# Optimization experiments

Hardware: AMD Instinct MI355X
Metric: run time of the kernel (lower is better)

The kernel has to match this reference:

```python
import jax, jax.numpy as jnp
import numpy as np
import math

LAMBDA_INIT = 0.8 - 0.6 * math.exp(-0.3 * 2)  # depth=2


def setup_inputs() -> dict:
    key = jax.random.key(0)
    ks = jax.random.split(key, 10)
    B, T, E, hd = 1, 2048, 1024, 32
    s = 0.02
    return {
        "x": jax.random.normal(ks[0], (B, T, E), jnp.float32),
        "Wq": jax.random.normal(ks[1], (E, E), jnp.float32) * s,
        "Wk": jax.random.normal(ks[2], (E, E), jnp.float32) * s,
        "Wv": jax.random.normal(ks[3], (E, E), jnp.float32) * s,
        "Wo": jax.random.normal(ks[4], (E, E), jnp.float32) * s,
        "lambda_q1": jax.random.normal(ks[5], (hd,), jnp.float32) * 0.1,
        "lambda_k1": jax.random.normal(ks[6], (hd,), jnp.float32) * 0.1,
        "lambda_q2": jax.random.normal(ks[7], (hd,), jnp.float32) * 0.1,
        "lambda_k2": jax.random.normal(ks[8], (hd,), jnp.float32) * 0.1,
        "gamma": jnp.ones((2 * hd,), jnp.float32),
    }


def reference(x, Wq, Wk, Wv, Wo, lambda_q1, lambda_k1, lambda_q2, lambda_k2, gamma):
    B, T, E = x.shape
    hd = gamma.shape[0] // 2          # head_dim
    H = E // (2 * hd)                 # num_heads
    scaling = hd ** -0.5

    # projections (torch Linear: y = x @ W.T)
    q = (x @ Wq.T).reshape(B, T, 2 * H, hd).transpose(0, 2, 1, 3)  # [B,2H,T,hd]
    k = (x @ Wk.T).reshape(B, T, 2 * H, hd).transpose(0, 2, 1, 3)  # [B,2H,T,hd]
    v = (x @ Wv.T).reshape(B, T, H, 2 * hd).transpose(0, 2, 1, 3)  # [B,H,T,2hd]

    # causal mask (offset = 0 since src_len == tgt_len)
    mask = jnp.triu(jnp.full((T, T), -jnp.inf, jnp.float32), k=1)

    attn_weights = jnp.einsum('bhtd,bhsd->bhts', q * scaling, k) + mask
    attn_weights = jax.nn.softmax(attn_weights.astype(jnp.float32), axis=-1).astype(x.dtype)

    lambda_1 = jnp.exp(jnp.sum(lambda_q1 * lambda_k1).astype(jnp.float32))
    lambda_2 = jnp.exp(jnp.sum(lambda_q2 * lambda_k2).astype(jnp.float32))
    lambda_full = (lambda_1 - lambda_2 + LAMBDA_INIT).astype(x.dtype)

    aw = attn_weights.reshape(B, H, 2, T, T)
    diff = aw[:, :, 0] - lambda_full * aw[:, :, 1]          # [B,H,T,T]

    attn = jnp.einsum('bhts,bhsd->bhtd', diff, v)            # [B,H,T,2hd]

    # RMSNorm over last dim (computed in fp32)
    a32 = attn.astype(jnp.float32)
    normed = a32 * jax.lax.rsqrt(jnp.mean(a32 * a32, axis=-1, keepdims=True) + 1e-5)
    attn = gamma * normed.astype(attn.dtype)
    attn = attn * (1 - LAMBDA_INIT)

    attn = attn.transpose(0, 2, 1, 3).reshape(B, T, E)
    return attn @ Wo.T
```

## Files before the change

### kernel.cpp

```cpp
#include <hip/hip_runtime.h>
#include <math.h>

typedef float f32x4 __attribute__((ext_vector_type(4)));
typedef __bf16 bf16x8 __attribute__((ext_vector_type(8)));

#define MFMA16(a, b, c) __builtin_amdgcn_mfma_f32_16x16x32_bf16((a), (b), (c), 0, 0, 0)

__device__ __forceinline__ unsigned short f2bf(float f) {
    union { float f; unsigned u; } v; v.f = f;
    return (unsigned short)((v.u + 0x7fffu + ((v.u >> 16) & 1u)) >> 16);
}
__device__ __forceinline__ unsigned pack2(float a, float b) {
    return (unsigned)f2bf(a) | ((unsigned)f2bf(b) << 16);
}

__global__ __launch_bounds__(256)
void convert_bf16(const float* __restrict__ x,  const float* __restrict__ wq,
                  const float* __restrict__ wk, const float* __restrict__ wv,
                  const float* __restrict__ wo,
                  unsigned short* __restrict__ xb,  unsigned short* __restrict__ wqb,
                  unsigned short* __restrict__ wkb, unsigned short* __restrict__ wvb,
                  unsigned short* __restrict__ wob)
{
    int i = blockIdx.x * 256 + threadIdx.x;
    const float* s; unsigned short* d; int o;
    if (i < 524288)       { s = x;  d = xb;  o = i; }
    else if (i < 786432)  { s = wq; d = wqb; o = i - 524288; }
    else if (i < 1048576) { s = wk; d = wkb; o = i - 786432; }
    else if (i < 1310720) { s = wv; d = wvb; o = i - 1048576; }
    else                  { s = wo; d = wob; o = i - 1310720; }
    float4 v = *reinterpret_cast<const float4*>(s + (size_t)o * 4);
    ushort4 r;
    r.x = f2bf(v.x); r.y = f2bf(v.y); r.z = f2bf(v.z); r.w = f2bf(v.w);
    *reinterpret_cast<ushort4*>(d + (size_t)o * 4) = r;
}

__device__ __forceinline__ void gemm_bf16_body(const unsigned short* __restrict__ A,
                                               const unsigned short* __restrict__ W,
                                               void* __restrict__ Cp, int mode)
{
    __shared__ char Al[128 * 128];
    __shared__ char Bl[64 * 128];

    const int tid = threadIdx.x;
    const int lane = tid & 63, w = tid >> 6;
    const int g = lane >> 4, r15 = lane & 15;
    const int wm = (w >> 1) * 64, wn = (w & 1) * 32;
    const int m0 = blockIdx.y * 128, n0 = blockIdx.x * 64;

    f32x4 acc[4][2] = {};
    bf16x8 ra[4], rb[2];

#pragma unroll
    for (int p = 0; p < 4; p++) {
        int idx = p * 256 + tid;
        int row = idx >> 3, c8 = idx & 7;
        ra[p] = *reinterpret_cast<const bf16x8*>(A + (size_t)(m0 + row) * 1024 + c8 * 8);
    }
#pragma unroll
    for (int p = 0; p < 2; p++) {
        int idx = p * 256 + tid;
        int row = idx >> 3, c8 = idx & 7;
        rb[p] = *reinterpret_cast<const bf16x8*>(W + (size_t)(n0 + row) * 1024 + c8 * 8);
    }

    for (int k0 = 0; k0 < 1024; k0 += 64) {
        __syncthreads();
#pragma unroll
        for (int p = 0; p < 4; p++) {
            int idx = p * 256 + tid;
            int row = idx >> 3, c8 = idx & 7;
            int byte = (row * 128 + c8 * 16) ^ ((row & 7) << 4);
            *reinterpret_cast<bf16x8*>(Al + byte) = ra[p];
        }
#pragma unroll
        for (int p = 0; p < 2; p++) {
            int idx = p * 256 + tid;
            int row = idx >> 3, c8 = idx & 7;
            int byte = (row * 128 + c8 * 16) ^ ((row & 7) << 4);
            *reinterpret_cast<bf16x8*>(Bl + byte) = rb[p];
        }
        if (k0 + 64 < 1024) {
#pragma unroll
            for (int p = 0; p < 4; p++) {
                int idx = p * 256 + tid;
                int row = idx >> 3, c8 = idx & 7;
                ra[p] = *reinterpret_cast<const bf16x8*>(A + (size_t)(m0 + row) * 1024 + k0 + 64 + c8 * 8);
            }
#pragma unroll
            for (int p = 0; p < 2; p++) {
                int idx = p * 256 + tid;
                int row = idx >> 3, c8 = idx & 7;
                rb[p] = *reinterpret_cast<const bf16x8*>(W + (size_t)(n0 + row) * 1024 + k0 + 64 + c8 * 8);
            }
        }
        __syncthreads();
#pragma unroll
        for (int c = 0; c < 2; c++) {
            bf16x8 af[4], bfr[2];
#pragma unroll
            for (int m = 0; m < 4; m++) {
                int row = wm + m * 16 + r15;
                int byte = (row * 128 + g * 16 + c * 64) ^ ((row & 7) << 4);
                af[m] = *reinterpret_cast<const bf16x8*>(Al + byte);
            }
#pragma unroll
            for (int n = 0; n < 2; n++) {
                int row = wn + n * 16 + r15;
                int byte = (row * 128 + g * 16 + c * 64) ^ ((row & 7) << 4);
                bfr[n] = *reinterpret_cast<const bf16x8*>(Bl + byte);
            }
#pragma unroll
            for (int m = 0; m < 4; m++)
#pragma unroll
                for (int n = 0; n < 2; n++)
                    acc[m][n] = MFMA16(af[m], bfr[n], acc[m][n]);
        }
    }

    if (mode == 0 || mode == 3) {
        const float cs = (mode == 3) ? 0.25504190132624806f : 1.0f;
        unsigned short* C = (unsigned short*)Cp;
#pragma unroll
        for (int m = 0; m < 4; m++)
#pragma unroll
            for (int n = 0; n < 2; n++)
#pragma unroll
                for (int i = 0; i < 4; i++)
                    C[(size_t)(m0 + wm + m * 16 + g * 4 + i) * 1024 + n0 + wn + n * 16 + r15] =
                        f2bf(acc[m][n][i] * cs);
    } else if (mode == 1) {
        unsigned short* C = (unsigned short*)Cp;
#pragma unroll
        for (int m = 0; m < 4; m++)
#pragma unroll
            for (int n = 0; n < 2; n++) {
                unsigned long long v = (unsigned long long)pack2(acc[m][n][0], acc[m][n][1])
                                     | ((unsigned long long)pack2(acc[m][n][2], acc[m][n][3]) << 32);
                *reinterpret_cast<unsigned long long*>(
                    C + (size_t)(n0 + wn + n * 16 + r15) * 2048 + m0 + wm + m * 16 + g * 4) = v;
            }
    } else {
        float* C = (float*)Cp;
#pragma unroll
        for (int m = 0; m < 4; m++)
#pragma unroll
            for (int n = 0; n < 2; n++)
#pragma unroll
                for (int i = 0; i < 4; i++)
                    C[(size_t)(m0 + wm + m * 16 + g * 4 + i) * 1024 + n0 + wn + n * 16 + r15] =
                        acc[m][n][i];
    }
}

__global__ __launch_bounds__(256)
void gemm_qkv_bf16(const unsigned short* __restrict__ xb, const unsigned short* __restrict__ wqb,
                   const unsigned short* __restrict__ wkb, const unsigned short* __restrict__ wvb,
                   unsigned short* __restrict__ Qb, unsigned short* __restrict__ Kb,
                   unsigned short* __restrict__ Vtb)
{
    int z = blockIdx.z;
    const unsigned short* W = (z == 0) ? wqb : (z == 1) ? wkb : wvb;
    void* C = (z == 0) ? (void*)Qb : (z == 1) ? (void*)Kb : (void*)Vtb;
    gemm_bf16_body(xb, W, C, (z == 2) ? 1 : (z == 0 ? 3 : 0));
}

__global__ __launch_bounds__(256)
void gemm_out_bf16(const unsigned short* __restrict__ Nb, const unsigned short* __restrict__ wob,
                   float* __restrict__ out)
{
    gemm_bf16_body(Nb, wob, out, 2);
}

__global__ __launch_bounds__(64, 3)
void attn_mfma3(const unsigned short* __restrict__ Qb, const unsigned short* __restrict__ Kb,
                const unsigned short* __restrict__ Vtb, unsigned short* __restrict__ Nb,
                const float* __restrict__ lq1, const float* __restrict__ lk1,
                const float* __restrict__ lq2, const float* __restrict__ lk2,
                const float* __restrict__ gamma)
{
    __shared__ char Pl[2][16 * 128];

    const int lane = threadIdx.x;
    const int g = lane >> 4, r15 = lane & 15;
    const int u = blockIdx.x >> 4, h = blockIdx.x & 15;
    const int qb = 127 - u;
    const int q0 = qb * 16;
    const int row_g = q0 + r15;

    float s1 = 0.f, s2 = 0.f;
#pragma unroll
    for (int i = 0; i < 32; i++) { s1 += lq1[i] * lk1[i]; s2 += lq2[i] * lk2[i]; }
    const float LI = 0.4707130183435841f;
    const float lam = expf(s1) - expf(s2) + LI;

    bf16x8 qf0 = *reinterpret_cast<const bf16x8*>(Qb + (size_t)row_g * 1024 + h * 64 + g * 8);
    bf16x8 qf1 = *reinterpret_cast<const bf16x8*>(Qb + (size_t)row_g * 1024 + h * 64 + 32 + g * 8);

    const unsigned short* Kh = Kb + h * 64;
    const unsigned short* Vh = Vtb + (size_t)(h * 64) * 2048;

    f32x4 oacc[2][4] = {};
    float m_u[2] = {-INFINITY, -INFINITY};
    float l_l[2] = {0.f, 0.f};

    const int nkb = (q0 + 79) >> 6;
    for (int kb = 0; kb < nkb; kb++) {
        const int j0 = kb * 64;

        bf16x8 ka0[4], ka1[4];
#pragma unroll
        for (int m = 0; m < 4; m++) {
            const unsigned short* kp = Kh + (size_t)(j0 + m * 16 + r15) * 1024 + g * 8;
            ka0[m] = *reinterpret_cast<const bf16x8*>(kp);
            ka1[m] = *reinterpret_cast<const bf16x8*>(kp + 32);
        }
        bf16x8 vf[4][2];
#pragma unroll
        for (int n = 0; n < 4; n++) {
            const unsigned short* vp = Vh + (size_t)(n * 16 + r15) * 2048 + j0 + g * 8;
            vf[n][0] = *reinterpret_cast<const bf16x8*>(vp);
            vf[n][1] = *reinterpret_cast<const bf16x8*>(vp + 32);
        }

        f32x4 sc0[4] = {}, sc1[4] = {};
#pragma unroll
        for (int m = 0; m < 4; m++) {
            sc0[m] = MFMA16(ka0[m], qf0, sc0[m]);
            sc1[m] = MFMA16(ka1[m], qf1, sc1[m]);
        }

        const bool diag = (kb == nkb - 1);
#pragma unroll
        for (int s = 0; s < 2; s++) {
            f32x4* sc = s ? sc1 : sc0;
            float sv[4][4];
            float mxl = -INFINITY;
            if (diag) {
#pragma unroll
                for (int m = 0; m < 4; m++)
#pragma unroll
                    for (int i = 0; i < 4; i++) {
                        float xv = ((j0 + m * 16 + g * 4 + i) <= row_g) ? sc[m][i] : -INFINITY;
                        sv[m][i] = xv;
                        mxl = fmaxf(mxl, xv);
                    }
            } else {
#pragma unroll
                for (int m = 0; m < 4; m++)
#pragma unroll
                    for (int i = 0; i < 4; i++) {
                        sv[m][i] = sc[m][i];
                        mxl = fmaxf(mxl, sc[m][i]);
                    }
            }
            if (__any(mxl > m_u[s] + 8.0f)) {
                float wm = mxl;
                wm = fmaxf(wm, __shfl_xor(wm, 1));
                wm = fmaxf(wm, __shfl_xor(wm, 2));
                wm = fmaxf(wm, __shfl_xor(wm, 4));
                wm = fmaxf(wm, __shfl_xor(wm, 8));
                wm = fmaxf(wm, __shfl_xor(wm, 16));
                wm = fmaxf(wm, __shfl_xor(wm, 32));
                const float corr = exp2f(m_u[s] - wm);
                m_u[s] = wm;
                l_l[s] *= corr;
#pragma unroll
                for (int n = 0; n < 4; n++)
#pragma unroll
                    for (int i = 0; i < 4; i++) oacc[s][n][i] *= corr;
            }
            float sum = 0.f;
#pragma unroll
            for (int m = 0; m < 4; m++) {
                float p0 = exp2f(sv[m][0] - m_u[s]);
                float p1 = exp2f(sv[m][1] - m_u[s]);
                float p2 = exp2f(sv[m][2] - m_u[s]);
                float p3 = exp2f(sv[m][3] - m_u[s]);
                sum += (p0 + p1) + (p2 + p3);
                unsigned long long pv = (unsigned long long)pack2(p0, p1)
                                      | ((unsigned long long)pack2(p2, p3) << 32);
                int byte = (r15 * 128 + m * 32 + g * 8) ^ ((r15 & 7) << 4);
                *reinterpret_cast<unsigned long long*>(Pl[s] + byte) = pv;
            }
            l_l[s] += sum;
        }

#pragma unroll
        for (int c = 0; c < 2; c++) {
            int pb = (r15 * 128 + g * 16 + c * 64) ^ ((r15 & 7) << 4);
            bf16x8 p0 = *reinterpret_cast<const bf16x8*>(Pl[0] + pb);
            bf16x8 p1 = *reinterpret_cast<const bf16x8*>(Pl[1] + pb);
#pragma unroll
            for (int n = 0; n < 4; n++) {
                oacc[0][n] = MFMA16(p0, vf[n][c], oacc[0][n]);
                oacc[1][n] = MFMA16(p1, vf[n][c], oacc[1][n]);
            }
        }
    }

    float l0 = l_l[0];
    l0 += __shfl_xor(l0, 16); l0 += __shfl_xor(l0, 32);
    float l1 = l_l[1];
    l1 += __shfl_xor(l1, 16); l1 += __shfl_xor(l1, 32);
    const float r1 = 1.f / l0;
    const float r2 = lam / l1;
    float i1[4], i2[4];
#pragma unroll
    for (int i = 0; i < 4; i++) {
        i1[i] = __shfl(r1, g * 4 + i);
        i2[i] = __shfl(r2, g * 4 + i);
    }
    float o[4][4], ss[4] = {0.f, 0.f, 0.f, 0.f};
#pragma unroll
    for (int n = 0; n < 4; n++)
#pragma unroll
        for (int i = 0; i < 4; i++) {
            float v = oacc[0][n][i] * i1[i] - oacc[1][n][i] * i2[i];
            o[n][i] = v;
            ss[i] = fmaf(v, v, ss[i]);
        }
#pragma unroll
    for (int i = 0; i < 4; i++) {
        ss[i] += __shfl_xor(ss[i], 1);
        ss[i] += __shfl_xor(ss[i], 2);
        ss[i] += __shfl_xor(ss[i], 4);
        ss[i] += __shfl_xor(ss[i], 8);
    }
    const float post = 1.f - LI;
    float gm4[4];
#pragma unroll
    for (int n = 0; n < 4; n++) gm4[n] = gamma[n * 16 + r15];
#pragma unroll
    for (int i = 0; i < 4; i++) {
        const float rs = rsqrtf(ss[i] * 0.015625f + 1e-5f);
#pragma unroll
        for (int n = 0; n < 4; n++) {
            Nb[(size_t)(q0 + g * 4 + i) * 1024 + h * 64 + n * 16 + r15] =
                f2bf(o[n][i] * rs * gm4[n] * post);
        }
    }
}

extern "C" void kernel_launch(void* const* d_in, const int* in_sizes, int n_in,
                              void* d_out, int out_size, void* d_ws, size_t ws_size,
                              hipStream_t stream)
{
    const float* x   = (const float*)d_in[0];
    const float* Wq  = (const float*)d_in[1];
    const float* Wk  = (const float*)d_in[2];
    const float* Wv  = (const float*)d_in[3];
    const float* Wo  = (const float*)d_in[4];
    const float* lq1 = (const float*)d_in[5];
    const float* lk1 = (const float*)d_in[6];
    const float* lq2 = (const float*)d_in[7];
    const float* lk2 = (const float*)d_in[8];
    const float* gm  = (const float*)d_in[9];
    float* out = (float*)d_out;

    unsigned short* ws  = (unsigned short*)d_ws;
    unsigned short* xb  = ws;
    unsigned short* wqb = xb  + 2097152;
    unsigned short* wkb = wqb + 1048576;
    unsigned short* wvb = wkb + 1048576;
    unsigned short* wob = wvb + 1048576;
    unsigned short* Qb  = wob + 1048576;
    unsigned short* Kb  = Qb  + 2097152;
    unsigned short* Vtb = Kb  + 2097152;
    unsigned short* Nb  = Vtb + 2097152;

    convert_bf16<<<6144, 256, 0, stream>>>(x, Wq, Wk, Wv, Wo, xb, wqb, wkb, wvb, wob);
    gemm_qkv_bf16<<<dim3(16, 16, 3), 256, 0, stream>>>(xb, wqb, wkb, wvb, Qb, Kb, Vtb);
    attn_mfma3<<<2048, 64, 0, stream>>>(Qb, Kb, Vtb, Nb, lq1, lk1, lq2, lk2, gm);
    gemm_out_bf16<<<dim3(16, 16), 256, 0, stream>>>(Nb, wob, out);
}
```

Before: 197.3 us.

## Prefetch next K tile in attention loop and use hardware bf16 pack

Restructures the attention kernel's key loop into a ping-pong, two-tile unrolled form. The next tile's K fragments are loaded into registers while the current tile's softmax and PV MFMAs run, hiding global load latency. It also swaps the software round-to-nearest bf16 packing for the v_cvt_pk_bf16_f32 instruction and lowers the launch-bounds occupancy hint from 3 to 2 waves. The trade is higher register pressure from the double-buffered K fragments and possibly lower occupancy.

```diff
diff --git a/kernel.cpp b/kernel.cpp
--- a/kernel.cpp
+++ b/kernel.cpp
@@ -12,6 +12,11 @@
 }
 __device__ __forceinline__ unsigned pack2(float a, float b) {
     return (unsigned)f2bf(a) | ((unsigned)f2bf(b) << 16);
+}
+__device__ __forceinline__ unsigned cvtpk_bf16(float lo, float hi) {
+    unsigned r;
+    asm("v_cvt_pk_bf16_f32 %0, %1, %2" : "=v"(r) : "v"(lo), "v"(hi));
+    return r;
 }
 
 __global__ __launch_bounds__(256)
@@ -172,8 +177,117 @@
     gemm_bf16_body(Nb, wob, out, 2);
 }
 
-__global__ __launch_bounds__(64, 3)
-void attn_mfma3(const unsigned short* __restrict__ Qb, const unsigned short* __restrict__ Kb,
+struct AttnState {
+    f32x4 oacc[2][4];
+    float m_u[2];
+    float l_l[2];
+};
+
+__device__ __forceinline__ void attn_tile(
+    int t, int nkb, int row_g, int g, int r15,
+    const unsigned short* __restrict__ Kh, const unsigned short* __restrict__ Vh,
+    bf16x8 (&kc0)[4], bf16x8 (&kc1)[4],
+    bf16x8 (&kn0)[4], bf16x8 (&kn1)[4],
+    const bf16x8& qf0, const bf16x8& qf1,
+    AttnState& st, char* __restrict__ Pl0, char* __restrict__ Pl1)
+{
+    const int j0 = t * 64;
+
+    bf16x8 vf[4][2];
+#pragma unroll
+    for (int n = 0; n < 4; n++) {
+        const unsigned short* vp = Vh + (size_t)(n * 16 + r15) * 2048 + j0 + g * 8;
+        vf[n][0] = *reinterpret_cast<const bf16x8*>(vp);
+        vf[n][1] = *reinterpret_cast<const bf16x8*>(vp + 32);
+    }
+
+    f32x4 sc0[4] = {}, sc1[4] = {};
+#pragma unroll
+    for (int m = 0; m < 4; m++) {
+        sc0[m] = MFMA16(kc0[m], qf0, sc0[m]);
+        sc1[m] = MFMA16(kc1[m], qf1, sc1[m]);
+    }
+
+    const int jn = ((t + 1 < nkb) ? t + 1 : t) * 64;
+#pragma unroll
+    for (int m = 0; m < 4; m++) {
+        const unsigned short* kp = Kh + (size_t)(jn + m * 16 + r15) * 1024 + g * 8;
+        kn0[m] = *reinterpret_cast<const bf16x8*>(kp);
+        kn1[m] = *reinterpret_cast<const bf16x8*>(kp + 32);
+    }
+
+    const bool diag = (t == nkb - 1);
+#pragma unroll
+    for (int s = 0; s < 2; s++) {
+        f32x4* sc = s ? sc1 : sc0;
+        char* Pl = s ? Pl1 : Pl0;
+        float sv[4][4];
+        float mxl = -INFINITY;
+        if (diag) {
+#pragma unroll
+            for (int m = 0; m < 4; m++)
+#pragma unroll
+                for (int i = 0; i < 4; i++) {
+                    float xv = ((j0 + m * 16 + g * 4 + i) <= row_g) ? sc[m][i] : -INFINITY;
+                    sv[m][i] = xv;
+                    mxl = fmaxf(mxl, xv);
+                }
+        } else {
+#pragma unroll
+            for (int m = 0; m < 4; m++)
+#pragma unroll
+                for (int i = 0; i < 4; i++) {
+                    sv[m][i] = sc[m][i];
+                    mxl = fmaxf(mxl, sc[m][i]);
+                }
+        }
+        if (__any(mxl > st.m_u[s] + 8.0f)) {
+            float wm = mxl;
+            wm = fmaxf(wm, __shfl_xor(wm, 1));
+            wm = fmaxf(wm, __shfl_xor(wm, 2));
+            wm = fmaxf(wm, __shfl_xor(wm, 4));
+            wm = fmaxf(wm, __shfl_xor(wm, 8));
+            wm = fmaxf(wm, __shfl_xor(wm, 16));
+            wm = fmaxf(wm, __shfl_xor(wm, 32));
+            const float corr = exp2f(st.m_u[s] - wm);
+            st.m_u[s] = wm;
+            st.l_l[s] *= corr;
+#pragma unroll
+            for (int n = 0; n < 4; n++)
+#pragma unroll
+                for (int i = 0; i < 4; i++) st.oacc[s][n][i] *= corr;
+        }
+        float sum = 0.f;
+#pragma unroll
+        for (int m = 0; m < 4; m++) {
+            float p0 = exp2f(sv[m][0] - st.m_u[s]);
+            float p1 = exp2f(sv[m][1] - st.m_u[s]);
+            float p2 = exp2f(sv[m][2] - st.m_u[s]);
+            float p3 = exp2f(sv[m][3] - st.m_u[s]);
+            sum += (p0 + p1) + (p2 + p3);
+            unsigned long long pv = (unsigned long long)cvtpk_bf16(p0, p1)
+                                  | ((unsigned long long)cvtpk_bf16(p2, p3) << 32);
+            int byte = (r15 * 128 + m * 32 + g * 8) ^ ((r15 & 7) << 4);
+            *reinterpret_cast<unsigned long long*>(Pl + byte) = pv;
+        }
+        st.l_l[s] += sum;
+    }
+
+#pragma unroll
+    for (int c = 0; c < 2; c++) {
+        int pb = (r15 * 128 + g * 16 + c * 64) ^ ((r15 & 7) << 4);
+        bf16x8 p0 = *reinterpret_cast<const bf16x8*>(Pl0 + pb);
+        bf16x8 p1 = *reinterpret_cast<const bf16x8*>(Pl1 + pb);
+#pragma unroll
+        for (int n = 0; n < 4; n++) {
+            st.oacc[0][n] = MFMA16(p0, vf[n][c], st.oacc[0][n]);
+            st.oacc[1][n] = MFMA16(p1, vf[n][c], st.oacc[1][n]);
+        }
+    }
+}
+
+__global__ __launch_bounds__(64, 2)
+void attn_mfma4(const unsigned short* __restrict__ Qb, const unsigned short* __restrict__ Kb,
                 const unsigned short* __restrict__ Vtb, unsigned short* __restrict__ Nb,
                 const float* __restrict__ lq1, const float* __restrict__ lk1,
                 const float* __restrict__ lq2, const float* __restrict__ lk2,
@@ -200,108 +314,35 @@
     const unsigned short* Kh = Kb + h * 64;
     const unsigned short* Vh = Vtb + (size_t)(h * 64) * 2048;
 
-    f32x4 oacc[2][4] = {};
-    float m_u[2] = {-INFINITY, -INFINITY};
-    float l_l[2] = {0.f, 0.f};
+    AttnState st;
+#pragma unroll
+    for (int s = 0; s < 2; s++) {
+        st.m_u[s] = -INFINITY; st.l_l[s] = 0.f;
+#pragma unroll
+        for (int n = 0; n < 4; n++) st.oacc[s][n] = (f32x4){0.f, 0.f, 0.f, 0.f};
+    }
 
     const int nkb = (q0 + 79) >> 6;
-    for (int kb = 0; kb < nkb; kb++) {
-        const int j0 = kb * 64;
-
-        bf16x8 ka0[4], ka1[4];
-#pragma unroll
-        for (int m = 0; m < 4; m++) {
-            const unsigned short* kp = Kh + (size_t)(j0 + m * 16 + r15) * 1024 + g * 8;
-            ka0[m] = *reinterpret_cast<const bf16x8*>(kp);
-            ka1[m] = *reinterpret_cast<const bf16x8*>(kp + 32);
-        }
-        bf16x8 vf[4][2];
-#pragma unroll
-        for (int n = 0; n < 4; n++) {
-            const unsigned short* vp = Vh + (size_t)(n * 16 + r15) * 2048 + j0 + g * 8;
-            vf[n][0] = *reinterpret_cast<const bf16x8*>(vp);
-            vf[n][1] = *reinterpret_cast<const bf16x8*>(vp + 32);
-        }
-
-        f32x4 sc0[4] = {}, sc1[4] = {};
-#pragma unroll
-        for (int m = 0; m < 4; m++) {
-            sc0[m] = MFMA16(ka0[m], qf0, sc0[m]);
-            sc1[m] = MFMA16(ka1[m], qf1, sc1[m]);
-        }
-
-        const bool diag = (kb == nkb - 1);
-#pragma unroll
-        for (int s = 0; s < 2; s++) {
-            f32x4* sc = s ? sc1 : sc0;
-            float sv[4][4];
-            float mxl = -INFINITY;
-            if (diag) {
-#pragma unroll
-                for (int m = 0; m < 4; m++)
-#pragma unroll
-                    for (int i = 0; i < 4; i++) {
-                        float xv = ((j0 + m * 16 + g * 4 + i) <= row_g) ? sc[m][i] : -INFINITY;
-                        sv[m][i] = xv;
-                        mxl = fmaxf(mxl, xv);
-                    }
-            } else {
-#pragma unroll
-                for (int m = 0; m < 4; m++)
-#pragma unroll
-                    for (int i = 0; i < 4; i++) {
-                        sv[m][i] = sc[m][i];
-                        mxl = fmaxf(mxl, sc[m][i]);
-                    }
-            }
-            if (__any(mxl > m_u[s] + 8.0f)) {
-                float wm = mxl;
-                wm = fmaxf(wm, __shfl_xor(wm, 1));
-                wm = fmaxf(wm, __shfl_xor(wm, 2));
-                wm = fmaxf(wm, __shfl_xor(wm, 4));
-                wm = fmaxf(wm, __shfl_xor(wm, 8));
-                wm = fmaxf(wm, __shfl_xor(wm, 16));
-                wm = fmaxf(wm, __shfl_xor(wm, 32));
-                const float corr = exp2f(m_u[s] - wm);
-                m_u[s] = wm;
-                l_l[s] *= corr;
-#pragma unroll
-                for (int n = 0; n < 4; n++)
-#pragma unroll
-                    for (int i = 0; i < 4; i++) oacc[s][n][i] *= corr;
-            }
-            float sum = 0.f;
-#pragma unroll
-            for (int m = 0; m < 4; m++) {
-                float p0 = exp2f(sv[m][0] - m_u[s]);
-                float p1 = exp2f(sv[m][1] - m_u[s]);
-                float p2 = exp2f(sv[m][2] - m_u[s]);
-                float p3 = exp2f(sv[m][3] - m_u[s]);
-                sum += (p0 + p1) + (p2 + p3);
-                unsigned long long pv = (unsigned long long)pack2(p0, p1)
-                                      | ((unsigned long long)pack2(p2, p3) << 32);
-                int byte = (r15 * 128 + m * 32 + g * 8) ^ ((r15 & 7) << 4);
-                *reinterpret_cast<unsigned long long*>(Pl[s] + byte) = pv;
-            }
-            l_l[s] += sum;
-        }
-
-#pragma unroll
-        for (int c = 0; c < 2; c++) {
-            int pb = (r15 * 128 + g * 16 + c * 64) ^ ((r15 & 7) << 4);
-            bf16x8 p0 = *reinterpret_cast<const bf16x8*>(Pl[0] + pb);
-            bf16x8 p1 = *reinterpret_cast<const bf16x8*>(Pl[1] + pb);
-#pragma unroll
-            for (int n = 0; n < 4; n++) {
-                oacc[0][n] = MFMA16(p0, vf[n][c], oacc[0][n]);
-                oacc[1][n] = MFMA16(p1, vf[n][c], oacc[1][n]);
-            }
-        }
-    }
-
-    float l0 = l_l[0];
+
+    bf16x8 kA0[4], kA1[4], kB0[4], kB1[4];
+#pragma unroll
+    for (int m = 0; m < 4; m++) {
+        const unsigned short* kp = Kh + (size_t)(m * 16 + r15) * 1024 + g * 8;
+        kA0[m] = *reinterpret_cast<const bf16x8*>(kp);
+        kA1[m] = *reinterpret_cast<const bf16x8*>(kp + 32);
+    }
+
+    for (int kb = 0; kb < nkb; kb += 2) {
+        attn_tile(kb, nkb, row_g, g, r15, Kh, Vh,
+                  kA0, kA1, kB0, kB1, qf0, qf1, st, Pl[0], Pl[1]);
+        if (kb + 1 < nkb)
+            attn_tile(kb + 1, nkb, row_g, g, r15, Kh, Vh,
+                      kB0, kB1, kA0, kA1, qf0, qf1, st, Pl[0], Pl[1]);
+    }
+
+    float l0 = st.l_l[0];
     l0 += __shfl_xor(l0, 16); l0 += __shfl_xor(l0, 32);
-    float l1 = l_l[1];
+    float l1 = st.l_l[1];
     l1 += __shfl_xor(l1, 16); l1 += __shfl_xor(l1, 32);
     const float r1 = 1.f / l0;
     const float r2 = lam / l1;
@@ -316,7 +357,7 @@
     for (int n = 0; n < 4; n++)
 #pragma unroll
         for (int i = 0; i < 4; i++) {
-            float v = oacc[0][n][i] * i1[i] - oacc[1][n][i] * i2[i];
+            float v = st.oacc[0][n][i] * i1[i] - st.oacc[1][n][i] * i2[i];
             o[n][i] = v;
             ss[i] = fmaf(v, v, ss[i]);
         }
@@ -371,6 +412,6 @@
 
     convert_bf16<<<6144, 256, 0, stream>>>(x, Wq, Wk, Wv, Wo, xb, wqb, wkb, wvb, wob);
     gemm_qkv_bf16<<<dim3(16, 16, 3), 256, 0, stream>>>(xb, wqb, wkb, wvb, Qb, Kb, Vtb);
-    attn_mfma3<<<2048, 64, 0, stream>>>(Qb, Kb, Vtb, Nb, lq1, lk1, lq2, lk2, gm);
+    attn_mfma4<<<2048, 64, 0, stream>>>(Qb, Kb, Vtb, Nb, lq1, lk1, lq2, lk2, gm);
     gemm_out_bf16<<<dim3(16, 16), 256, 0, stream>>>(Nb, wob, out);
 }
```

Result: faster. 190.0 us (-3.7%).
